# Kernel optimization log

Hardware: AMD Instinct MI355X
Metric: run time of the kernel (lower is better)

The kernel has to match this reference:

```python
import jax, jax.numpy as jnp
import numpy as np
import math

BL, N, T, C, H = 16, 256, 32, 256, 4
HD = C // H
GEOM_DIM = 12
K_REL = 32
LN_EPS = 1e-5
GEPS = 1e-6
NEG = -1e9


def setup_inputs() -> dict:
    key = jax.random.key(0)
    ks = jax.random.split(key, 24)
    s = 0.02  # weight init scale
    d = {
        "x": jax.random.normal(ks[0], (BL, N, C), jnp.float32),
        "lang_fea": jax.random.normal(ks[1], (BL, T, C), jnp.float32),
        "centers": jax.random.normal(ks[2], (BL, N, 3), jnp.float32),
        "corners": jax.random.normal(ks[3], (BL, N, 8, 3), jnp.float32),
        "obj_mask": jnp.ones((BL, N), dtype=bool),
        # LayerNorm
        "ln_g": jnp.ones((C,), jnp.float32),
        "ln_b": jnp.zeros((C,), jnp.float32),
        # qkv / proj
        "W_qkv": s * jax.random.normal(ks[4], (C, 3 * C), jnp.float32),
        "b_qkv": jnp.zeros((3 * C,), jnp.float32),
        "W_proj": s * jax.random.normal(ks[5], (C, C), jnp.float32),
        "b_proj": jnp.zeros((C,), jnp.float32),
        # geom2bias MLP (12 -> C -> H)
        "Wg1": s * jax.random.normal(ks[6], (GEOM_DIM, C), jnp.float32),
        "bg1": jnp.zeros((C,), jnp.float32),
        "Wg2": s * jax.random.normal(ks[7], (C, H), jnp.float32),
        "bg2": jnp.zeros((H,), jnp.float32),
        # txt2head MLP (C -> C -> H)
        "Wt1": s * jax.random.normal(ks[8], (C, C), jnp.float32),
        "bt1": jnp.zeros((C,), jnp.float32),
        "Wt2": s * jax.random.normal(ks[9], (C, H), jnp.float32),
        "bt2": jnp.zeros((H,), jnp.float32),
        "alpha": jnp.float32(0.05),
    }
    return d


def _build_relation_geom(centers, corners):
    # centers: (BL,N,3), corners: (BL,N,8,3) -> (BL,N,N,12)
    rel_vec = centers[:, None, :, :] - centers[:, :, None, :]  # (BL,N,N,3) j - i
    dist = jnp.linalg.norm(rel_vec, axis=-1, keepdims=True)
    horiz_dist = jnp.linalg.norm(rel_vec[..., :2], axis=-1, keepdims=True)
    delta_z = rel_vec[..., 2:3]
    cos_elev = delta_z / (dist + GEPS)
    sizes = corners.max(axis=2) - corners.min(axis=2)  # (BL,N,3)
    size_i = sizes[:, :, None, :]
    size_j = sizes[:, None, :, :]
    size_diff = size_j - size_i
    size_ratio = size_j / (size_i + GEPS)
    return jnp.concatenate([rel_vec, dist, horiz_dist, cos_elev, size_diff, size_ratio], axis=-1)


def _knn_mask(centers, k):
    # (BL,N,N) bool: each row i keeps its k nearest columns j (incl. self)
    diff = centers[:, :, None, :] - centers[:, None, :, :]
    dist = jnp.linalg.norm(diff, axis=-1)  # (BL,N,N)
    _, idx = jax.lax.top_k(-dist, k)  # smallest-k indices, (BL,N,k)
    return jnp.any(jax.nn.one_hot(idx, dist.shape[-1], dtype=bool), axis=-2)


def reference(x, lang_fea, centers, corners, obj_mask, ln_g, ln_b,
              W_qkv, b_qkv, W_proj, b_proj, Wg1, bg1, Wg2, bg2,
              Wt1, bt1, Wt2, bt2, alpha):
    # geometric pairwise bias: (BL,N,N,12) -> MLP -> (BL,H,N,N)
    geom = _build_relation_geom(centers, corners)
    bias = jax.nn.gelu(geom @ Wg1 + bg1, approximate=False) @ Wg2 + bg2
    bias = jnp.transpose(bias, (0, 3, 1, 2))  # (BL,H,N,N)

    # language-conditioned head gate: (BL,H,1,1)
    sent = lang_fea.mean(axis=1)  # (BL,C)
    head_w = jax.nn.sigmoid(jax.nn.gelu(sent @ Wt1 + bt1, approximate=False) @ Wt2 + bt2)
    head_w = head_w[:, :, None, None]

    warm = 1.0  # epoch=None -> no warmup scaling

    knn_mask = _knn_mask(centers, K_REL)
    pair = obj_mask[:, :, None] & obj_mask[:, None, :]
    attn_mask = knn_mask & pair  # (BL,N,N)

    residual = x
    # LayerNorm
    mu = x.mean(axis=-1, keepdims=True)
    var = x.var(axis=-1, keepdims=True)
    xn = (x - mu) * jax.lax.rsqrt(var + LN_EPS) * ln_g + ln_b

    qkv = (xn @ W_qkv + b_qkv).reshape(BL, N, 3, H, HD)
    q = jnp.transpose(qkv[:, :, 0], (0, 2, 1, 3))  # (BL,H,N,HD)
    k = jnp.transpose(qkv[:, :, 1], (0, 2, 1, 3))
    v = jnp.transpose(qkv[:, :, 2], (0, 2, 1, 3))

    logits = jnp.einsum("bhid,bhjd->bhij", q, k) / math.sqrt(HD)
    bias_eff = warm * alpha * head_w * bias
    logits = logits + bias_eff
    logits = jnp.where(attn_mask[:, None, :, :], logits, NEG)

    attn = jax.nn.softmax(logits, axis=-1)  # dropout is identity at eval
    out = jnp.einsum("bhij,bhjd->bhid", attn, v)
    out = jnp.transpose(out, (0, 2, 1, 3)).reshape(BL, N, C)
    out = out @ W_proj + b_proj
    x_out = residual + out
    return (x_out, jax.lax.stop_gradient(attn), jax.lax.stop_gradient(bias_eff))
```

## Files before the change

kernel.cpp:

```cpp
#include <hip/hip_runtime.h>
#include <math.h>

#define BLn 16
#define Nn 256
#define Tn 32
#define Cn 256
#define Hn 4
#define HDn 64
#define KREL 32

typedef float f32x4 __attribute__((ext_vector_type(4)));
typedef __bf16 bf16x8 __attribute__((ext_vector_type(8)));
typedef _Float16 f16x4 __attribute__((ext_vector_type(4)));
typedef _Float16 f16x2 __attribute__((ext_vector_type(2)));

#define MFMA16(a, b, c) __builtin_amdgcn_mfma_f32_16x16x32_bf16(a, b, c, 0, 0, 0)
#define MFMA16H(a, b, c) __builtin_amdgcn_mfma_f32_16x16x16f16(a, b, c, 0, 0, 0)

__device__ __forceinline__ float gelu_exact(float x) {
    return 0.5f * x * (1.0f + erff(x * 0.70710678118654752440f));
}

__device__ __forceinline__ f16x2 gelu_pk(f16x2 x) {
    const f16x2 P4 = {(_Float16)4.0f, (_Float16)4.0f};
    const f16x2 M4 = {(_Float16)-4.0f, (_Float16)-4.0f};
    const f16x2 C0 = {(_Float16)0.833076f, (_Float16)0.833076f};
    const f16x2 C1 = {(_Float16)-0.139388f, (_Float16)-0.139388f};
    const f16x2 C2 = {(_Float16)0.013040f, (_Float16)0.013040f};
    const f16x2 C3 = {(_Float16)-0.000413f, (_Float16)-0.000413f};
    const f16x2 HF = {(_Float16)0.5f, (_Float16)0.5f};
    const f16x2 ONE = {(_Float16)1.0f, (_Float16)1.0f};
    const f16x2 ZERO = {(_Float16)0.0f, (_Float16)0.0f};
    f16x2 xc = __builtin_elementwise_min(__builtin_elementwise_max(x, M4), P4);
    f16x2 v = xc * xc;
    f16x2 w = C3 * v + C2;
    w = w * v + C1;
    w = w * v + C0;
    f16x2 t = w * xc;
    f16x2 s = t * HF + HF;
    s = __builtin_elementwise_min(__builtin_elementwise_max(s, ZERO), ONE);
    return x * s;
}

__global__ void __launch_bounds__(256) k_prep(
    const float* __restrict__ x, const float* __restrict__ ln_g, const float* __restrict__ ln_b,
    __bf16* __restrict__ xnb, const float* __restrict__ centers, const int* __restrict__ obj,
    unsigned char* __restrict__ knn, const float* __restrict__ corners,
    float* __restrict__ sizes, const float* __restrict__ lang, const float* __restrict__ Wt1,
    const float* __restrict__ bt1, const float* __restrict__ Wt2, const float* __restrict__ bt2,
    float* __restrict__ headw, const float* __restrict__ W_qkv, __bf16* __restrict__ wqT,
    const float* __restrict__ W_proj, __bf16* __restrict__ wpT) {
    __shared__ float4 d4[64];
    __shared__ float sm1[Nn];
    __shared__ float T[64][65];
    float* sm0 = (float*)d4;
    int blk = blockIdx.x;
    int tid = threadIdx.x;

    if (blk < 1024) {
        int row = blk * 4 + (tid >> 6);
        int l = tid & 63;
        float4 v = ((const float4*)(x + (size_t)row * Cn))[l];
        float s = v.x + v.y + v.z + v.w;
        float q = v.x * v.x + v.y * v.y + v.z * v.z + v.w * v.w;
        for (int m = 32; m > 0; m >>= 1) {
            s += __shfl_xor(s, m, 64);
            q += __shfl_xor(q, m, 64);
        }
        float mu = s * (1.0f / Cn);
        float var = q * (1.0f / Cn) - mu * mu;
        float r = rsqrtf(var + 1e-5f);
        float4 g = ((const float4*)ln_g)[l];
        float4 be = ((const float4*)ln_b)[l];
        __bf16 ob[4];
        ob[0] = (__bf16)((v.x - mu) * r * g.x + be.x);
        ob[1] = (__bf16)((v.y - mu) * r * g.y + be.y);
        ob[2] = (__bf16)((v.z - mu) * r * g.z + be.z);
        ob[3] = (__bf16)((v.w - mu) * r * g.w + be.w);
        *(uint2*)(xnb + (size_t)row * Cn + l * 4) = *(uint2*)ob;
    } else if (blk < 5120) {
        int bi = blk - 1024;
        int b = bi >> 8, i = bi & 255;
        int j = tid;
        float cx = centers[(b * Nn + i) * 3 + 0];
        float cy = centers[(b * Nn + i) * 3 + 1];
        float cz = centers[(b * Nn + i) * 3 + 2];
        float dx = centers[(b * Nn + j) * 3 + 0] - cx;
        float dy = centers[(b * Nn + j) * 3 + 1] - cy;
        float dz = centers[(b * Nn + j) * 3 + 2] - cz;
        float dd = sqrtf(dx * dx + dy * dy + dz * dz);
        sm0[j] = dd;
        __syncthreads();
        int rank = 0;
        for (int t4 = 0; t4 < 64; t4++) {
            float4 o = d4[t4];
            int t = t4 * 4;
            rank += (o.x < dd) || (o.x == dd && t + 0 < j);
            rank += (o.y < dd) || (o.y == dd && t + 1 < j);
            rank += (o.z < dd) || (o.z == dd && t + 2 < j);
            rank += (o.w < dd) || (o.w == dd && t + 3 < j);
        }
        bool m = (rank < KREL);
        m = m && (obj[b * Nn + i] != 0) && (obj[b * Nn + j] != 0);
        knn[(size_t)bi * Nn + j] = m ? 1 : 0;
    } else if (blk < 5136) {
        int b = blk - 5120, n = tid;
        const float* p = corners + (size_t)((b * Nn + n) * 8) * 3;
        float mn[3] = {1e30f, 1e30f, 1e30f}, mx[3] = {-1e30f, -1e30f, -1e30f};
        for (int v = 0; v < 8; v++)
            for (int d = 0; d < 3; d++) {
                float t = p[v * 3 + d];
                mn[d] = fminf(mn[d], t);
                mx[d] = fmaxf(mx[d], t);
            }
        for (int d = 0; d < 3; d++) sizes[(b * Nn + n) * 3 + d] = mx[d] - mn[d];
    } else if (blk < 5152) {
        int b = blk - 5136, c = tid;
        float s = 0.0f;
        for (int t = 0; t < Tn; t++) s += lang[((size_t)b * Tn + t) * Cn + c];
        sm0[c] = s * (1.0f / Tn);
        __syncthreads();
        float acc = bt1[c];
        for (int i = 0; i < Cn; i++) acc += sm0[i] * Wt1[i * Cn + c];
        sm1[c] = gelu_exact(acc);
        __syncthreads();
        if (c < Hn) {
            float a = bt2[c];
            for (int i = 0; i < Cn; i++) a += sm1[i] * Wt2[i * Hn + c];
            headw[b * Hn + c] = 1.0f / (1.0f + expf(-a));
        }
    } else if (blk < 5200) {
        int t = blk - 5152;
        int kt = t & 3, ot = t >> 2;
        for (int itr = 0; itr < 16; itr++) {
            int idx = itr * 256 + tid;
            int r = idx >> 6, c = idx & 63;
            T[r][c] = W_qkv[(size_t)(kt * 64 + r) * 768 + ot * 64 + c];
        }
        __syncthreads();
        for (int itr = 0; itr < 16; itr++) {
            int idx = itr * 256 + tid;
            int r = idx >> 6, c = idx & 63;
            wqT[(size_t)(ot * 64 + r) * 256 + kt * 64 + c] = (__bf16)T[c][r];
        }
    } else {
        int t = blk - 5200;
        int kt = t & 3, ot = t >> 2;
        for (int itr = 0; itr < 16; itr++) {
            int idx = itr * 256 + tid;
            int r = idx >> 6, c = idx & 63;
            T[r][c] = W_proj[(size_t)(kt * 64 + r) * 256 + ot * 64 + c];
        }
        __syncthreads();
        for (int itr = 0; itr < 16; itr++) {
            int idx = itr * 256 + tid;
            int r = idx >> 6, c = idx & 63;
            wpT[(size_t)(ot * 64 + r) * 256 + kt * 64 + c] = (__bf16)T[c][r];
        }
    }
}

__global__ void __launch_bounds__(256, 4) k_heavy(
    const float* __restrict__ centers, const float* __restrict__ sizes,
    const float* __restrict__ Wg1, const float* __restrict__ bg1,
    const float* __restrict__ Wg2, const float* __restrict__ bg2,
    const float* __restrict__ headw, const float* __restrict__ alphap,
    float* __restrict__ bias_eff, const __bf16* __restrict__ xnb,
    const __bf16* __restrict__ wqT, const float* __restrict__ bqkv,
    __bf16* __restrict__ qkvb) {
    __shared__ __align__(16) _Float16 fT[Nn][20];
    __shared__ __align__(16) _Float16 W1T[Cn][20];
    __shared__ __align__(16) _Float16 W2T[16][264];

    int blk = blockIdx.x;
    int tid = threadIdx.x;

    if (blk >= 4096) {
        int t = blk - 4096;
        int ib = t & 63, y = t >> 6;
        int w = tid >> 6, l = tid & 63, lr = l & 15, lg = l >> 4;
        const __bf16* arow = xnb + (size_t)(ib * 64 + w * 16 + lr) * Cn;

        f32x4 acc[4];
#pragma unroll
        for (int ot = 0; ot < 4; ot++) acc[ot] = (f32x4){0.f, 0.f, 0.f, 0.f};
#pragma unroll
        for (int kc = 0; kc < 8; kc++) {
            bf16x8 af = *(const bf16x8*)(arow + kc * 32 + lg * 8);
#pragma unroll
            for (int ot = 0; ot < 4; ot++) {
                bf16x8 bfr = *(const bf16x8*)(wqT + (size_t)(y * 64 + ot * 16 + lr) * Cn +
                                              kc * 32 + lg * 8);
                acc[ot] = MFMA16(af, bfr, acc[ot]);
            }
        }
        int seg = y >> 2, h = y & 3;
        __bf16* segp = qkvb + (size_t)seg * 1048576;
#pragma unroll
        for (int ot = 0; ot < 4; ot++) {
            float bo = bqkv[y * 64 + ot * 16 + lr];
#pragma unroll
            for (int r = 0; r < 4; r++) {
                int ig = ib * 64 + w * 16 + lg * 4 + r;
                int b = ig >> 8, n = ig & 255;
                segp[(((size_t)(b * Hn + h)) * Nn + n) * HDn + ot * 16 + lr] =
                    (__bf16)(acc[ot][r] + bo);
            }
        }
        return;
    }

    int b = blk >> 8, i = blk & 255;

    {
        int c = tid;
        _Float16 t1[20];
#pragma unroll
        for (int k = 0; k < 12; k++) t1[k] = (_Float16)Wg1[k * Cn + c];
        t1[12] = (_Float16)bg1[c];
#pragma unroll
        for (int k = 13; k < 20; k++) t1[k] = (_Float16)0.f;
#pragma unroll
        for (int q = 0; q < 5; q++) *(uint2*)&W1T[c][q * 4] = *(uint2*)&t1[q * 4];
#pragma unroll
        for (int h = 0; h < 16; h++)
            W2T[h][c] = (h < Hn) ? (_Float16)Wg2[c * Hn + h] : (_Float16)0.f;
    }
    {
        int j = tid;
        float ci0 = centers[(b * Nn + i) * 3 + 0];
        float ci1 = centers[(b * Nn + i) * 3 + 1];
        float ci2 = centers[(b * Nn + i) * 3 + 2];
        float si0 = sizes[(b * Nn + i) * 3 + 0];
        float si1 = sizes[(b * Nn + i) * 3 + 1];
        float si2 = sizes[(b * Nn + i) * 3 + 2];
        float cj0 = centers[(b * Nn + j) * 3 + 0];
        float cj1 = centers[(b * Nn + j) * 3 + 1];
        float cj2 = centers[(b * Nn + j) * 3 + 2];
        float sj0 = sizes[(b * Nn + j) * 3 + 0];
        float sj1 = sizes[(b * Nn + j) * 3 + 1];
        float sj2 = sizes[(b * Nn + j) * 3 + 2];
        float rx = cj0 - ci0, ry = cj1 - ci1, rz = cj2 - ci2;
        float h2 = rx * rx + ry * ry;
        float dist = sqrtf(h2 + rz * rz);
        float horiz = sqrtf(h2);
        float f[16];
        f[0] = rx; f[1] = ry; f[2] = rz;
        f[3] = dist; f[4] = horiz;
        f[5] = rz / (dist + 1e-6f);
        f[6] = sj0 - si0; f[7] = sj1 - si1; f[8] = sj2 - si2;
        f[9] = sj0 / (si0 + 1e-6f);
        f[10] = sj1 / (si1 + 1e-6f);
        f[11] = sj2 / (si2 + 1e-6f);
        f[12] = 1.0f;
        _Float16 tf[20];
#pragma unroll
        for (int k = 0; k < 13; k++) tf[k] = (_Float16)f[k];
#pragma unroll
        for (int k = 13; k < 20; k++) tf[k] = (_Float16)0.f;
#pragma unroll
        for (int q = 0; q < 5; q++) *(uint2*)&fT[j][q * 4] = *(uint2*)&tf[q * 4];
    }
    __syncthreads();

    int w = tid >> 6, l = tid & 63;
    int lr = l & 15, lg = l >> 4;
    int jw = w * 64;

    f32x4 zero4 = {0.f, 0.f, 0.f, 0.f};

    f16x4 bf_[4];
#pragma unroll
    for (int jt = 0; jt < 4; jt++) bf_[jt] = *(const f16x4*)&fT[jw + jt * 16 + lr][lg * 4];

    f32x4 pacc[4];
#pragma unroll
    for (int jt = 0; jt < 4; jt++) pacc[jt] = zero4;

#pragma unroll 2
    for (int cw = 0; cw < 16; cw++) {
        int cbase = cw * 16;
        f16x4 aw = *(const f16x4*)&W1T[cbase + lr][lg * 4];
        f16x4 b2 = *(const f16x4*)&W2T[lr][cbase + lg * 4];
#pragma unroll
        for (int jt = 0; jt < 4; jt++) {
            f32x4 acc = MFMA16H(aw, bf_[jt], zero4);
            f16x2 h01 = __builtin_bit_cast(f16x2, __builtin_amdgcn_cvt_pkrtz(acc[0], acc[1]));
            f16x2 h23 = __builtin_bit_cast(f16x2, __builtin_amdgcn_cvt_pkrtz(acc[2], acc[3]));
            h01 = gelu_pk(h01);
            h23 = gelu_pk(h23);
            f16x4 ga;
            ga[0] = h01[0]; ga[1] = h01[1]; ga[2] = h23[0]; ga[3] = h23[1];
            pacc[jt] = MFMA16H(ga, b2, pacc[jt]);
        }
    }

    float alpha = alphap[0];
    if (lr < Hn) {
        float hw_ = headw[b * Hn + lr];
        float bg = bg2[lr];
        float* dst = bias_eff + (((size_t)(b * Hn + lr)) * Nn + i) * Nn;
#pragma unroll
        for (int jt = 0; jt < 4; jt++) {
            f32x4 o4;
#pragma unroll
            for (int r = 0; r < 4; r++) o4[r] = alpha * hw_ * (pacc[jt][r] + bg);
            *(f32x4*)&dst[jw + jt * 16 + lg * 4] = o4;
        }
    }
}

__global__ void __launch_bounds__(256) k_attn(const __bf16* __restrict__ qkvb,
                                              const float* __restrict__ bias_eff,
                                              const unsigned char* __restrict__ knn,
                                              float* __restrict__ attn_out,
                                              __bf16* __restrict__ houtb) {
    __shared__ __bf16 Vt[64][264];
    __shared__ __bf16 Plds[4][16][136];
    int blk = blockIdx.x;
    int bh = blk >> 2, it = blk & 3;
    int b = bh >> 2, h = bh & 3;
    int tid = threadIdx.x;

    const __bf16* vbase = qkvb + 2 * 1048576 + (size_t)bh * (Nn * HDn);
    {
        int j = tid;
#pragma unroll
        for (int c8 = 0; c8 < 8; c8++) {
            bf16x8 v8 = *(const bf16x8*)(vbase + (size_t)j * HDn + c8 * 8);
#pragma unroll
            for (int e = 0; e < 8; e++) Vt[c8 * 8 + e][j] = v8[e];
        }
    }
    __syncthreads();

    int w = tid >> 6, l = tid & 63;
    int lr = l & 15, lg = l >> 4;
    int i_glob = it * 64 + w * 16 + lr;

    const __bf16* qrow = qkvb + (size_t)bh * (Nn * HDn) + (size_t)i_glob * HDn;
    bf16x8 qf0 = *(const bf16x8*)(qrow + lg * 8);
    bf16x8 qf1 = *(const bf16x8*)(qrow + 32 + lg * 8);

    const __bf16* kbase = qkvb + 1048576 + (size_t)bh * (Nn * HDn);
    f32x4 s[16];
#pragma unroll
    for (int jt = 0; jt < 16; jt++) {
        const __bf16* krow = kbase + (size_t)(jt * 16 + lr) * HDn;
        bf16x8 ka = *(const bf16x8*)(krow + lg * 8);
        bf16x8 kb = *(const bf16x8*)(krow + 32 + lg * 8);
        f32x4 acc = (f32x4){0.f, 0.f, 0.f, 0.f};
        acc = MFMA16(ka, qf0, acc);
        acc = MFMA16(kb, qf1, acc);
        s[jt] = acc;
    }

    const float* brow = bias_eff + ((size_t)bh * Nn + i_glob) * Nn;
    const unsigned int* mrow = (const unsigned int*)(knn + ((size_t)(b * Nn + i_glob)) * Nn);
    float mx = -1e30f;
#pragma unroll
    for (int jt = 0; jt < 16; jt++) {
        f32x4 bi = *(const f32x4*)(brow + jt * 16 + lg * 4);
        unsigned int mk = mrow[jt * 4 + lg];
#pragma unroll
        for (int r = 0; r < 4; r++) {
            float v = fmaf(s[jt][r], 0.125f, bi[r]);
            v = ((mk >> (8 * r)) & 0xff) ? v : -1e9f;
            s[jt][r] = v;
            mx = fmaxf(mx, v);
        }
    }
    mx = fmaxf(mx, __shfl_xor(mx, 16, 64));
    mx = fmaxf(mx, __shfl_xor(mx, 32, 64));
    float sum = 0.0f;
#pragma unroll
    for (int jt = 0; jt < 16; jt++)
#pragma unroll
        for (int r = 0; r < 4; r++) {
            float e = __builtin_amdgcn_exp2f((s[jt][r] - mx) * 1.44269504f);
            s[jt][r] = e;
            sum += e;
        }
    sum += __shfl_xor(sum, 16, 64);
    sum += __shfl_xor(sum, 32, 64);
    float inv = 1.0f / sum;

    float* arow = attn_out + ((size_t)bh * Nn + i_glob) * Nn;
#pragma unroll
    for (int jt = 0; jt < 16; jt++) {
        f32x4 o4;
#pragma unroll
        for (int r = 0; r < 4; r++) {
            float a = s[jt][r] * inv;
            s[jt][r] = a;
            o4[r] = a;
        }
        *(f32x4*)(arow + jt * 16 + lg * 4) = o4;
    }

    f32x4 o[4];
#pragma unroll
    for (int dt = 0; dt < 4; dt++) o[dt] = (f32x4){0.f, 0.f, 0.f, 0.f};
    for (int half = 0; half < 2; half++) {
#pragma unroll
        for (int jr = 0; jr < 8; jr++) {
            int jt = half * 8 + jr;
            __bf16 pb[4];
#pragma unroll
            for (int r = 0; r < 4; r++) pb[r] = (__bf16)s[jt][r];
            *(uint2*)&Plds[w][lr][jr * 16 + lg * 4] = *(uint2*)pb;
        }
#pragma unroll
        for (int kk = 0; kk < 4; kk++) {
            bf16x8 pfrag = *(const bf16x8*)&Plds[w][lr][kk * 32 + lg * 8];
#pragma unroll
            for (int dt = 0; dt < 4; dt++) {
                bf16x8 vfrag = *(const bf16x8*)&Vt[dt * 16 + lr][half * 128 + kk * 32 + lg * 8];
                o[dt] = MFMA16(vfrag, pfrag, o[dt]);
            }
        }
    }

    __bf16* hrow = houtb + ((size_t)(b * Nn + i_glob)) * Cn + h * HDn;
#pragma unroll
    for (int dt = 0; dt < 4; dt++) {
        __bf16 hb[4];
#pragma unroll
        for (int r = 0; r < 4; r++) hb[r] = (__bf16)o[dt][r];
        *(uint2*)(hrow + dt * 16 + lg * 4) = *(uint2*)hb;
    }
}

__global__ void __launch_bounds__(256) k_proj(const __bf16* __restrict__ houtb,
                                              const __bf16* __restrict__ wpT,
                                              const float* __restrict__ bp,
                                              const float* __restrict__ x,
                                              float* __restrict__ xout) {
    int ib = blockIdx.x, y = blockIdx.y;
    int tid = threadIdx.x;
    int w = tid >> 6, l = tid & 63, lr = l & 15, lg = l >> 4;
    const __bf16* arow = houtb + (size_t)(ib * 64 + w * 16 + lr) * Cn;

    f32x4 acc[4];
#pragma unroll
    for (int ot = 0; ot < 4; ot++) acc[ot] = (f32x4){0.f, 0.f, 0.f, 0.f};
#pragma unroll
    for (int kc = 0; kc < 8; kc++) {
        bf16x8 af = *(const bf16x8*)(arow + kc * 32 + lg * 8);
#pragma unroll
        for (int ot = 0; ot < 4; ot++) {
            bf16x8 bfr = *(const bf16x8*)(wpT + (size_t)(y * 64 + ot * 16 + lr) * Cn +
                                          kc * 32 + lg * 8);
            acc[ot] = MFMA16(af, bfr, acc[ot]);
        }
    }
#pragma unroll
    for (int ot = 0; ot < 4; ot++) {
        int o = y * 64 + ot * 16 + lr;
        float bo = bp[o];
#pragma unroll
        for (int r = 0; r < 4; r++) {
            int ig = ib * 64 + w * 16 + lg * 4 + r;
            size_t idx = (size_t)ig * Cn + o;
            xout[idx] = x[idx] + bo + acc[ot][r];
        }
    }
}

extern "C" void kernel_launch(void* const* d_in, const int* in_sizes, int n_in,
                              void* d_out, int out_size, void* d_ws, size_t ws_size,
                              hipStream_t stream) {
    const float* x       = (const float*)d_in[0];
    const float* lang    = (const float*)d_in[1];
    const float* centers = (const float*)d_in[2];
    const float* corners = (const float*)d_in[3];
    const int*   obj     = (const int*)d_in[4];
    const float* ln_g    = (const float*)d_in[5];
    const float* ln_b    = (const float*)d_in[6];
    const float* W_qkv   = (const float*)d_in[7];
    const float* b_qkv   = (const float*)d_in[8];
    const float* W_proj  = (const float*)d_in[9];
    const float* b_proj  = (const float*)d_in[10];
    const float* Wg1     = (const float*)d_in[11];
    const float* bg1     = (const float*)d_in[12];
    const float* Wg2     = (const float*)d_in[13];
    const float* bg2     = (const float*)d_in[14];
    const float* Wt1     = (const float*)d_in[15];
    const float* bt1     = (const float*)d_in[16];
    const float* Wt2     = (const float*)d_in[17];
    const float* bt2     = (const float*)d_in[18];
    const float* alpha   = (const float*)d_in[19];

    float* out = (float*)d_out;
    float* xout     = out;
    float* attn     = out + 1048576;
    float* bias_eff = out + 5242880;

    __bf16* xnb   = (__bf16*)d_ws;
    __bf16* qkvb  = xnb + 1048576;
    __bf16* houtb = qkvb + 3145728;
    __bf16* wqT   = houtb + 1048576;
    __bf16* wpT   = wqT + 196608;
    float*  sizes = (float*)(wpT + 65536);
    float*  headw = sizes + 12288;
    unsigned char* knn = (unsigned char*)(headw + 64);

    k_prep<<<5216, 256, 0, stream>>>(x, ln_g, ln_b, xnb, centers, obj, knn, corners, sizes,
                                     lang, Wt1, bt1, Wt2, bt2, headw, W_qkv, wqT, W_proj, wpT);
    k_heavy<<<4864, 256, 0, stream>>>(centers, sizes, Wg1, bg1, Wg2, bg2, headw, alpha,
                                      bias_eff, xnb, wqT, b_qkv, qkvb);
    k_attn<<<256, 256, 0, stream>>>(qkvb, bias_eff, knn, attn, houtb);
    k_proj<<<dim3(64, 4), 256, 0, stream>>>(houtb, wpT, b_proj, x, xout);
}
```

Baseline: 120.2 us.

## Fuse output projection into attention kernel and store V pre-transposed

The QKV GEMM now writes V transposed (d-major) via an LDS staging tile, so the attention kernel reads V fragments straight from global memory instead of transposing V into shared memory. The attention grid is remapped so each block handles 16 query rows for all four heads (one head per wave). The per-row head outputs are gathered in LDS and the output projection plus residual is done in the same kernel, which removes the separate k_proj launch and the houtb round trip. In exchange, V fragments now come from global/L2 rather than LDS, and the block needs a barrier before the projection.

Result: slower. 127.9 us (+6.4%).

```diff
diff --git a/kernel.cpp b/kernel.cpp
--- a/kernel.cpp
+++ b/kernel.cpp
@@ -195,17 +195,40 @@
             }
         }
         int seg = y >> 2, h = y & 3;
-        __bf16* segp = qkvb + (size_t)seg * 1048576;
-#pragma unroll
-        for (int ot = 0; ot < 4; ot++) {
-            float bo = bqkv[y * 64 + ot * 16 + lr];
-#pragma unroll
-            for (int r = 0; r < 4; r++) {
-                int ig = ib * 64 + w * 16 + lg * 4 + r;
-                int b = ig >> 8, n = ig & 255;
-                segp[(((size_t)(b * Hn + h)) * Nn + n) * HDn + ot * 16 + lr] =
-                    (__bf16)(acc[ot][r] + bo);
+        int bq = ib >> 2;
+        if (seg < 2) {
+            __bf16* segp = qkvb + (size_t)seg * 1048576;
+#pragma unroll
+            for (int ot = 0; ot < 4; ot++) {
+                float bo = bqkv[y * 64 + ot * 16 + lr];
+#pragma unroll
+                for (int r = 0; r < 4; r++) {
+                    int ig = ib * 64 + w * 16 + lg * 4 + r;
+                    int n = ig & 255;
+                    segp[(((size_t)(bq * Hn + h)) * Nn + n) * HDn + ot * 16 + lr] =
+                        (__bf16)(acc[ot][r] + bo);
+                }
             }
+        } else {
+            __bf16(*Vl)[72] = (__bf16(*)[72])fT;
+            int nloc = w * 16 + lg * 4;
+#pragma unroll
+            for (int ot = 0; ot < 4; ot++) {
+                int d = ot * 16 + lr;
+                float bo = bqkv[y * 64 + d];
+                __bf16 pb[4];
+#pragma unroll
+                for (int r = 0; r < 4; r++) pb[r] = (__bf16)(acc[ot][r] + bo);
+                *(uint2*)&Vl[d][nloc] = *(uint2*)pb;
+            }
+            __syncthreads();
+            int d = tid >> 2, q = tid & 3;
+            __bf16* vT = qkvb + 2 * 1048576 + (size_t)(bq * Hn + h) * (HDn * Nn);
+            int ncol = ((ib & 3) * 64) + q * 16;
+            uint4 a0 = *(uint4*)&Vl[d][q * 16];
+            uint4 a1 = *(uint4*)&Vl[d][q * 16 + 8];
+            *(uint4*)(vT + (size_t)d * Nn + ncol) = a0;
+            *(uint4*)(vT + (size_t)d * Nn + ncol + 8) = a1;
         }
         return;
     }
@@ -314,31 +337,22 @@
                                               const float* __restrict__ bias_eff,
                                               const unsigned char* __restrict__ knn,
                                               float* __restrict__ attn_out,
-                                              __bf16* __restrict__ houtb) {
-    __shared__ __bf16 Vt[64][264];
+                                              const __bf16* __restrict__ wpT,
+                                              const float* __restrict__ bp,
+                                              const float* __restrict__ x,
+                                              float* __restrict__ xout) {
     __shared__ __bf16 Plds[4][16][136];
+    __shared__ __bf16 htile[16][264];
     int blk = blockIdx.x;
-    int bh = blk >> 2, it = blk & 3;
-    int b = bh >> 2, h = bh & 3;
+    int b = blk >> 4, it = blk & 15;
     int tid = threadIdx.x;
-
-    const __bf16* vbase = qkvb + 2 * 1048576 + (size_t)bh * (Nn * HDn);
-    {
-        int j = tid;
-#pragma unroll
-        for (int c8 = 0; c8 < 8; c8++) {
-            bf16x8 v8 = *(const bf16x8*)(vbase + (size_t)j * HDn + c8 * 8);
-#pragma unroll
-            for (int e = 0; e < 8; e++) Vt[c8 * 8 + e][j] = v8[e];
-        }
-    }
-    __syncthreads();
-
     int w = tid >> 6, l = tid & 63;
     int lr = l & 15, lg = l >> 4;
-    int i_glob = it * 64 + w * 16 + lr;
-
-    const __bf16* qrow = qkvb + (size_t)bh * (Nn * HDn) + (size_t)i_glob * HDn;
+    int h = w;
+    int bh = b * Hn + h;
+    int i = it * 16 + lr;
+
+    const __bf16* qrow = qkvb + (size_t)bh * (Nn * HDn) + (size_t)i * HDn;
     bf16x8 qf0 = *(const bf16x8*)(qrow + lg * 8);
     bf16x8 qf1 = *(const bf16x8*)(qrow + 32 + lg * 8);
 
@@ -355,8 +369,8 @@
         s[jt] = acc;
     }
 
-    const float* brow = bias_eff + ((size_t)bh * Nn + i_glob) * Nn;
-    const unsigned int* mrow = (const unsigned int*)(knn + ((size_t)(b * Nn + i_glob)) * Nn);
+    const float* brow = bias_eff + ((size_t)bh * Nn + i) * Nn;
+    const unsigned int* mrow = (const unsigned int*)(knn + ((size_t)(b * Nn + i)) * Nn);
     float mx = -1e30f;
 #pragma unroll
     for (int jt = 0; jt < 16; jt++) {
@@ -385,7 +399,7 @@
     sum += __shfl_xor(sum, 32, 64);
     float inv = 1.0f / sum;
 
-    float* arow = attn_out + ((size_t)bh * Nn + i_glob) * Nn;
+    float* arow = attn_out + ((size_t)bh * Nn + i) * Nn;
 #pragma unroll
     for (int jt = 0; jt < 16; jt++) {
         f32x4 o4;
@@ -398,6 +412,7 @@
         *(f32x4*)(arow + jt * 16 + lg * 4) = o4;
     }
 
+    const __bf16* vT = qkvb + 2 * 1048576 + (size_t)bh * (HDn * Nn);
     f32x4 o[4];
 #pragma unroll
     for (int dt = 0; dt < 4; dt++) o[dt] = (f32x4){0.f, 0.f, 0.f, 0.f};
@@ -415,54 +430,44 @@
             bf16x8 pfrag = *(const bf16x8*)&Plds[w][lr][kk * 32 + lg * 8];
 #pragma unroll
             for (int dt = 0; dt < 4; dt++) {
-                bf16x8 vfrag = *(const bf16x8*)&Vt[dt * 16 + lr][half * 128 + kk * 32 + lg * 8];
+                bf16x8 vfrag = *(const bf16x8*)(vT + (size_t)(dt * 16 + lr) * Nn + half * 128 +
+                                                kk * 32 + lg * 8);
                 o[dt] = MFMA16(vfrag, pfrag, o[dt]);
             }
         }
     }
 
-    __bf16* hrow = houtb + ((size_t)(b * Nn + i_glob)) * Cn + h * HDn;
 #pragma unroll
     for (int dt = 0; dt < 4; dt++) {
         __bf16 hb[4];
 #pragma unroll
         for (int r = 0; r < 4; r++) hb[r] = (__bf16)o[dt][r];
-        *(uint2*)(hrow + dt * 16 + lg * 4) = *(uint2*)hb;
-    }
-}
-
-__global__ void __launch_bounds__(256) k_proj(const __bf16* __restrict__ houtb,
-                                              const __bf16* __restrict__ wpT,
-                                              const float* __restrict__ bp,
-                                              const float* __restrict__ x,
-                                              float* __restrict__ xout) {
-    int ib = blockIdx.x, y = blockIdx.y;
-    int tid = threadIdx.x;
-    int w = tid >> 6, l = tid & 63, lr = l & 15, lg = l >> 4;
-    const __bf16* arow = houtb + (size_t)(ib * 64 + w * 16 + lr) * Cn;
-
-    f32x4 acc[4];
-#pragma unroll
-    for (int ot = 0; ot < 4; ot++) acc[ot] = (f32x4){0.f, 0.f, 0.f, 0.f};
+        *(uint2*)&htile[lr][h * HDn + dt * 16 + lg * 4] = *(uint2*)hb;
+    }
+    __syncthreads();
+
+    f32x4 pa[4];
+#pragma unroll
+    for (int ot = 0; ot < 4; ot++) pa[ot] = (f32x4){0.f, 0.f, 0.f, 0.f};
 #pragma unroll
     for (int kc = 0; kc < 8; kc++) {
-        bf16x8 af = *(const bf16x8*)(arow + kc * 32 + lg * 8);
+        bf16x8 af = *(const bf16x8*)&htile[lr][kc * 32 + lg * 8];
 #pragma unroll
         for (int ot = 0; ot < 4; ot++) {
-            bf16x8 bfr = *(const bf16x8*)(wpT + (size_t)(y * 64 + ot * 16 + lr) * Cn +
+            bf16x8 bfr = *(const bf16x8*)(wpT + (size_t)(w * 64 + ot * 16 + lr) * Cn +
                                           kc * 32 + lg * 8);
-            acc[ot] = MFMA16(af, bfr, acc[ot]);
+            pa[ot] = MFMA16(af, bfr, pa[ot]);
         }
     }
 #pragma unroll
     for (int ot = 0; ot < 4; ot++) {
-        int o = y * 64 + ot * 16 + lr;
-        float bo = bp[o];
+        int oc = w * 64 + ot * 16 + lr;
+        float bo = bp[oc];
 #pragma unroll
         for (int r = 0; r < 4; r++) {
-            int ig = ib * 64 + w * 16 + lg * 4 + r;
-            size_t idx = (size_t)ig * Cn + o;
-            xout[idx] = x[idx] + bo + acc[ot][r];
+            int rowg = b * Nn + it * 16 + lg * 4 + r;
+            size_t idx = (size_t)rowg * Cn + oc;
+            xout[idx] = x[idx] + bo + pa[ot][r];
         }
     }
 }
@@ -498,8 +503,7 @@
 
     __bf16* xnb   = (__bf16*)d_ws;
     __bf16* qkvb  = xnb + 1048576;
-    __bf16* houtb = qkvb + 3145728;
-    __bf16* wqT   = houtb + 1048576;
+    __bf16* wqT   = qkvb + 3145728;
     __bf16* wpT   = wqT + 196608;
     float*  sizes = (float*)(wpT + 65536);
     float*  headw = sizes + 12288;
@@ -509,6 +513,5 @@
                                      lang, Wt1, bt1, Wt2, bt2, headw, W_qkv, wqT, W_proj, wpT);
     k_heavy<<<4864, 256, 0, stream>>>(centers, sizes, Wg1, bg1, Wg2, bg2, headw, alpha,
                                       bias_eff, xnb, wqT, b_qkv, qkvb);
-    k_attn<<<256, 256, 0, stream>>>(qkvb, bias_eff, knn, attn, houtb);
-    k_proj<<<dim3(64, 4), 256, 0, stream>>>(houtb, wpT, b_proj, x, xout);
+    k_attn<<<256, 256, 0, stream>>>(qkvb, bias_eff, knn, attn, wpT, b_proj, x, xout);
 }
```
